# Performance work log

Measured on AMD Instinct MI355X. Metric: run time of the kernel, lower is better.

Reference implementation:

```python
import jax, jax.numpy as jnp
import numpy as np

SEQ, BATCH, D, N = 256, 4, 512, 32768
TEMP = 0.5


def setup_inputs() -> dict:
    key = jax.random.key(0)
    ks = jax.random.split(key, 16)
    d = D
    # xavier_uniform with gain 1/sqrt(2) for square [d,d]: limit = gain*sqrt(6/(d+d))
    lim_t = (1.0 / np.sqrt(2.0)) * np.sqrt(6.0 / (d + d))
    lim_g1 = np.sqrt(6.0 / (2 * d + d))  # default kaiming-ish scale approximated by xavier
    lim_g2 = np.sqrt(6.0 / (d + 1))
    inp = {
        "q": jax.random.normal(ks[0], (SEQ, BATCH, D), dtype=jnp.float32),
        "prev_layer_output": jax.random.normal(ks[1], (SEQ, BATCH, D), dtype=jnp.float32),
        "Wq": jax.random.uniform(ks[2], (D, D), jnp.float32, -lim_t, lim_t),
        "bq": jnp.zeros((D,), jnp.float32),
        "Wk": jax.random.uniform(ks[3], (D, D), jnp.float32, -lim_t, lim_t),
        "bk": jnp.zeros((D,), jnp.float32),
        "Wv": jax.random.uniform(ks[4], (D, D), jnp.float32, -lim_t, lim_t),
        "bv": jnp.zeros((D,), jnp.float32),
        "Wg1": jax.random.uniform(ks[5], (D, 2 * D), jnp.float32, -lim_g1, lim_g1),
        "bg1": jnp.zeros((D,), jnp.float32),
        "Wg2": jax.random.uniform(ks[6], (1, D), jnp.float32, -lim_g2, lim_g2),
        "bg2": jnp.zeros((1,), jnp.float32),
        "dstore_k": jax.random.normal(ks[7], (N, D), dtype=jnp.float32),
        "dstore_v": jax.random.normal(ks[8], (N, D), dtype=jnp.float32),
    }
    return inp


def reference(q, prev_layer_output, Wq, bq, Wk, bk, Wv, bv, Wg1, bg1, Wg2, bg2, dstore_k, dstore_v):
    # [S,B,D] -> [B,S,D]
    qb = jnp.transpose(q, (1, 0, 2))
    prevb = jnp.transpose(prev_layer_output, (1, 0, 2))
    # enable_tune projections
    _q = qb @ Wq.T + bq                      # [B,S,D]
    _k = dstore_k @ Wk.T + bk                # [N,D]
    _v = dstore_v @ Wv.T + bv                # [N,D]
    _q = _q * (D ** -0.5)
    # attention over datastore, temperature-scaled softmax
    logits = jnp.einsum("bsd,nd->bsn", _q, _k) / TEMP  # [B,S,N]
    w = jax.nn.softmax(logits, axis=-1)
    attn = jnp.einsum("bsn,nd->bsd", w, _v)            # [B,S,D]
    # gated residual fusion
    cat = jnp.concatenate([attn, prevb], axis=-1)      # [B,S,2D]
    h = jax.nn.relu(cat @ Wg1.T + bg1)                 # [B,S,D]
    sigma = jax.nn.sigmoid(h @ Wg2.T + bg2)            # [B,S,1]
    res = attn * sigma + prevb * (1.0 - sigma)
    return jnp.transpose(res, (1, 0, 2))               # [S,B,D]
```

## Files before the change

### kernel.cpp

```cpp
#include <hip/hip_runtime.h>
#include <hip/hip_bf16.h>
#include <cstdint>
#include <cstddef>


typedef unsigned short u16;
typedef u16    u16x8 __attribute__((ext_vector_type(8)));
typedef u16    u16x4 __attribute__((ext_vector_type(4)));
typedef __bf16 bf16x8 __attribute__((ext_vector_type(8)));
typedef float  f32x4 __attribute__((ext_vector_type(4)));

#define MFMA16(a, b, c) __builtin_amdgcn_mfma_f32_16x16x32_bf16( \
    __builtin_bit_cast(bf16x8, (a)), __builtin_bit_cast(bf16x8, (b)), (c), 0, 0, 0)

__device__ __forceinline__ u16 f2bf(float f) {
  unsigned u = __builtin_bit_cast(unsigned, f);
  u += 0x7fffu + ((u >> 16) & 1u);
  return (u16)(u >> 16);
}

__global__ __launch_bounds__(256) void prep_cvt(const float* __restrict__ src,
                                                u16* __restrict__ dst) {
  size_t i = ((size_t)blockIdx.x * 256 + threadIdx.x) * 4;
  float4 v = *(const float4*)(src + i);
  u16x4 o = {f2bf(v.x), f2bf(v.y), f2bf(v.z), f2bf(v.w)};
  *(u16x4*)(dst + i) = o;
}

__global__ __launch_bounds__(256) void prep_vt(const float* __restrict__ v,
                                               u16* __restrict__ vt) {
  __shared__ u16 Lt[64 * 72];
  const int n0 = blockIdx.x * 64, d0 = blockIdx.y * 64;
  const int t = threadIdx.x;
  const int n = t >> 2, c4 = t & 3;
#pragma unroll
  for (int i = 0; i < 4; i++) {
    int col = (c4 + 4 * i) * 4;
    float4 x = *(const float4*)(v + (size_t)(n0 + n) * 512 + d0 + col);
    Lt[(col + 0) * 72 + n] = f2bf(x.x);
    Lt[(col + 1) * 72 + n] = f2bf(x.y);
    Lt[(col + 2) * 72 + n] = f2bf(x.z);
    Lt[(col + 3) * 72 + n] = f2bf(x.w);
  }
  __syncthreads();
#pragma unroll
  for (int u = 0; u < 2; u++) {
    int unit = t + 256 * u;
    int d = unit >> 3, un = unit & 7;
    *(u16x8*)(vt + (size_t)(d0 + d) * 32768 + n0 + un * 8) =
        *(const u16x8*)&Lt[d * 72 + un * 8];
  }
}

template <bool TRANSB, bool CONCAT, bool RELU, bool OUTBF16, bool ROWSCALE,
          bool CQ, bool GATE, int KK>
__global__ __launch_bounds__(256, 2) void gemm64(
    const float* __restrict__ A, const float* __restrict__ A2,
    const float* __restrict__ B, const float* __restrict__ bias,
    const float* __restrict__ lvec, const float* __restrict__ bkv,
    const float* __restrict__ wg2, float alpha, void* __restrict__ Cv,
    float* __restrict__ cqout, float* __restrict__ sdot) {
  __shared__ u16 As[64 * 72];
  __shared__ u16 Bs[64 * 72];
  const int tid = threadIdx.x;
  const int w = tid >> 6, lane = tid & 63, quad = lane >> 4, l15 = lane & 15;
  const int m0 = blockIdx.y * 64, n0 = blockIdx.x * 64;
  const int arow = tid >> 2, ac4 = tid & 3;
  float rs = 1.0f;
  if (ROWSCALE) rs = 1.0f / lvec[m0 + arow];
  const bool docq = CQ && (blockIdx.x == 0);
  float cqacc = 0.f;
  const f32x4 fzero = {0.f, 0.f, 0.f, 0.f};
  f32x4 acc[4];
#pragma unroll
  for (int i = 0; i < 4; i++) acc[i] = fzero;

  float4 ra[4], rb[4], rk[4];
  auto loadA = [&](int k0) {
    const float* src;
    if (CONCAT)
      src = (k0 < 512) ? (A + (size_t)(m0 + arow) * 512 + k0)
                       : (A2 + (size_t)(m0 + arow) * 512 + (k0 - 512));
    else
      src = A + (size_t)(m0 + arow) * KK + k0;
#pragma unroll
    for (int i = 0; i < 4; i++) ra[i] = *(const float4*)(src + (ac4 + 4 * i) * 4);
  };
  auto loadB = [&](int k0) {
    const float* src = TRANSB ? (B + (size_t)(n0 + arow) * KK + k0)
                              : (B + (size_t)(k0 + arow) * 512 + n0);
#pragma unroll
    for (int i = 0; i < 4; i++) rb[i] = *(const float4*)(src + (ac4 + 4 * i) * 4);
  };
  auto loadK = [&](int k0) {
#pragma unroll
    for (int i = 0; i < 4; i++) rk[i] = *(const float4*)(bkv + k0 + (ac4 + 4 * i) * 4);
  };

  loadA(0); loadB(0);
  if (docq) loadK(0);
#pragma unroll
  for (int k0 = 0; k0 < KK; k0 += 64) {
    __syncthreads();
#pragma unroll
    for (int i = 0; i < 4; i++) {
      int col = (ac4 + 4 * i) * 4;
      float4 x = ra[i];
      if (ROWSCALE) { x.x *= rs; x.y *= rs; x.z *= rs; x.w *= rs; }
      u16x4 oa = {f2bf(x.x), f2bf(x.y), f2bf(x.z), f2bf(x.w)};
      *(u16x4*)&As[arow * 72 + col] = oa;
      float4 y = rb[i];
      if (TRANSB) {
        u16x4 ob = {f2bf(y.x), f2bf(y.y), f2bf(y.z), f2bf(y.w)};
        *(u16x4*)&Bs[arow * 72 + col] = ob;
      } else {
        Bs[(col + 0) * 72 + arow] = f2bf(y.x);
        Bs[(col + 1) * 72 + arow] = f2bf(y.y);
        Bs[(col + 2) * 72 + arow] = f2bf(y.z);
        Bs[(col + 3) * 72 + arow] = f2bf(y.w);
      }
      if (docq)
        cqacc += ra[i].x * rk[i].x + ra[i].y * rk[i].y + ra[i].z * rk[i].z +
                 ra[i].w * rk[i].w;
    }
    if (k0 + 64 < KK) {
      loadA(k0 + 64); loadB(k0 + 64);
      if (docq) loadK(k0 + 64);
    }
    __syncthreads();
#pragma unroll
    for (int ks = 0; ks < 2; ks++) {
      u16x8 af = *(const u16x8*)&As[(w * 16 + l15) * 72 + ks * 32 + quad * 8];
#pragma unroll
      for (int nt = 0; nt < 4; nt++) {
        u16x8 bf = *(const u16x8*)&Bs[(nt * 16 + l15) * 72 + ks * 32 + quad * 8];
        acc[nt] = MFMA16(af, bf, acc[nt]);
      }
    }
  }

  if (docq) {
    cqacc += __shfl_xor(cqacc, 1, 64);
    cqacc += __shfl_xor(cqacc, 2, 64);
    if (ac4 == 0) cqout[m0 + arow] = alpha * cqacc;
  }
  if (GATE) {
    float part[4] = {0.f, 0.f, 0.f, 0.f};
#pragma unroll
    for (int nt = 0; nt < 4; nt++) {
      int col = n0 + nt * 16 + l15;
      float b = bias[col], wv = wg2[col];
#pragma unroll
      for (int i = 0; i < 4; i++) {
        float y = fmaxf((acc[nt][i] + b) * alpha, 0.f);
        part[i] += y * wv;
      }
    }
#pragma unroll
    for (int i = 0; i < 4; i++) {
      float v = part[i];
      v += __shfl_xor(v, 1, 64); v += __shfl_xor(v, 2, 64);
      v += __shfl_xor(v, 4, 64); v += __shfl_xor(v, 8, 64);
      if (l15 == 0) atomicAdd(&sdot[m0 + w * 16 + quad * 4 + i], v);
    }
  } else {
#pragma unroll
    for (int nt = 0; nt < 4; nt++) {
      int col = n0 + nt * 16 + l15;
      float b = bias ? bias[col] : 0.f;
#pragma unroll
      for (int i = 0; i < 4; i++) {
        int row = m0 + w * 16 + quad * 4 + i;
        float y = (acc[nt][i] + b) * alpha;
        if (RELU) y = fmaxf(y, 0.f);
        if (OUTBF16)
          ((u16*)Cv)[(size_t)row * 512 + col] = f2bf(y);
        else
          ((float*)Cv)[(size_t)row * 512 + col] = y;
      }
    }
  }
}

__global__ __launch_bounds__(512, 2) void flash(
    const u16* __restrict__ kbf,
    const u16* __restrict__ vt,
    const u16* __restrict__ q2,
    const float* __restrict__ cq,
    float* __restrict__ racc,
    float* __restrict__ lacc) {
  __shared__ u16 Ks[32 * 520];
  __shared__ u16 Es[2][64 * 40];
  const int tid = threadIdx.x;
  const int w = tid >> 6, lane = tid & 63, quad = lane >> 4, l15 = lane & 15;
  const int bx = blockIdx.x;
  const int xcd = bx & 7, idx = bx >> 3;
  const int qt = idx & 15, nh2 = idx >> 4;
  const int rowbase = xcd * 4096 + nh2 * 2048;
  const int qbase = qt * 64;
  const int qg = w >> 1, nh = w & 1;
  const int colb = w * 64;

  u16x8 qf[16];
  {
    const u16* qp = q2 + (size_t)(qbase + qg * 16 + l15) * 512 + quad * 8;
#pragma unroll
    for (int ks = 0; ks < 16; ks++) qf[ks] = *(const u16x8*)(qp + ks * 32);
  }
  float cq4[4];
#pragma unroll
  for (int i = 0; i < 4; i++) cq4[i] = cq[qbase + qg * 16 + quad * 4 + i];
  float lp[4] = {0.f, 0.f, 0.f, 0.f};
  const f32x4 fzero = {0.f, 0.f, 0.f, 0.f};
  f32x4 acc[4][4];
#pragma unroll
  for (int a = 0; a < 4; a++)
#pragma unroll
    for (int b = 0; b < 4; b++) acc[a][b] = fzero;

  u16x8 st[4];
  u16x8 bvp[4];
#pragma unroll
  for (int u = 0; u < 4; u++) {
    int flat = tid + u * 512;
    st[u] = *(const u16x8*)(kbf + (size_t)(rowbase + (flat >> 6)) * 512 + (flat & 63) * 8);
  }

#pragma unroll 1
  for (int sub = 0; sub < 64; ++sub) {
    const int n0 = rowbase + sub * 32;
    __syncthreads();
#pragma unroll
    for (int u = 0; u < 4; u++) {
      int flat = tid + u * 512;
      *(u16x8*)&Ks[(flat >> 6) * 520 + (flat & 63) * 8] = st[u];
    }
    if (sub + 1 < 64) {
      int n1 = n0 + 32;
#pragma unroll
      for (int u = 0; u < 4; u++) {
        int flat = tid + u * 512;
        st[u] = *(const u16x8*)(kbf + (size_t)(n1 + (flat >> 6)) * 512 + (flat & 63) * 8);
      }
    }
    if (sub > 0) {
      const u16* eb = Es[(sub - 1) & 1];
      u16x8 ef[4];
#pragma unroll
      for (int q2i = 0; q2i < 4; q2i++)
        ef[q2i] = *(const u16x8*)&eb[(q2i * 16 + l15) * 40 + quad * 8];
#pragma unroll
      for (int ct = 0; ct < 4; ct++)
#pragma unroll
        for (int q2i = 0; q2i < 4; q2i++)
          acc[q2i][ct] = MFMA16(ef[q2i], bvp[ct], acc[q2i][ct]);
    }
    __syncthreads();
#pragma unroll
    for (int ct = 0; ct < 4; ct++)
      bvp[ct] = *(const u16x8*)(vt + (size_t)(colb + ct * 16 + l15) * 32768 + n0 + quad * 8);
    f32x4 s = fzero;
#pragma unroll
    for (int ks = 0; ks < 16; ks++) {
      u16x8 bfg = *(const u16x8*)&Ks[(nh * 16 + l15) * 520 + ks * 32 + quad * 8];
      s = MFMA16(qf[ks], bfg, s);
    }
    u16* ew = Es[sub & 1];
#pragma unroll
    for (int i = 0; i < 4; i++) {
      float e = __expf(s[i] + cq4[i]);
      lp[i] += e;
      ew[(qg * 16 + quad * 4 + i) * 40 + nh * 16 + l15] = f2bf(e);
    }
  }
  __syncthreads();
  {
    const u16* eb = Es[1];
    u16x8 ef[4];
#pragma unroll
    for (int q2i = 0; q2i < 4; q2i++)
      ef[q2i] = *(const u16x8*)&eb[(q2i * 16 + l15) * 40 + quad * 8];
#pragma unroll
    for (int ct = 0; ct < 4; ct++)
#pragma unroll
      for (int q2i = 0; q2i < 4; q2i++)
        acc[q2i][ct] = MFMA16(ef[q2i], bvp[ct], acc[q2i][ct]);
  }
#pragma unroll
  for (int q2i = 0; q2i < 4; q2i++)
#pragma unroll
    for (int ct = 0; ct < 4; ct++) {
      int col = colb + ct * 16 + l15;
#pragma unroll
      for (int i = 0; i < 4; i++) {
        int row = qbase + q2i * 16 + quad * 4 + i;
        atomicAdd(&racc[(size_t)row * 512 + col], acc[q2i][ct][i]);
      }
    }
#pragma unroll
  for (int i = 0; i < 4; i++) {
    float v = lp[i];
#pragma unroll
    for (int off = 1; off < 16; off <<= 1) v += __shfl_xor(v, off, 64);
    if (l15 == 0) atomicAdd(&lacc[qbase + qg * 16 + quad * 4 + i], v);
  }
}

__global__ __launch_bounds__(128) void finalize(
    const float* __restrict__ sdot, const float* __restrict__ bg2,
    const float* __restrict__ attn, const float* __restrict__ prev,
    float* __restrict__ out) {
  int r = blockIdx.x, t = threadIdx.x;
  float sg = 1.f / (1.f + __expf(-(sdot[r] + bg2[0])));
  float4 a = ((const float4*)(attn + (size_t)r * 512))[t];
  float4 p = ((const float4*)(prev + (size_t)r * 512))[t];
  float4 o = {a.x * sg + p.x * (1.f - sg), a.y * sg + p.y * (1.f - sg),
              a.z * sg + p.z * (1.f - sg), a.w * sg + p.w * (1.f - sg)};
  ((float4*)(out + (size_t)r * 512))[t] = o;
}

extern "C" void kernel_launch(void* const* d_in, const int* in_sizes, int n_in,
                              void* d_out, int out_size, void* d_ws, size_t ws_size,
                              hipStream_t stream) {
  const float* q    = (const float*)d_in[0];
  const float* prev = (const float*)d_in[1];
  const float* Wq   = (const float*)d_in[2];
  const float* bq   = (const float*)d_in[3];
  const float* Wk   = (const float*)d_in[4];
  const float* bk   = (const float*)d_in[5];
  const float* Wv   = (const float*)d_in[6];
  const float* bv   = (const float*)d_in[7];
  const float* Wg1  = (const float*)d_in[8];
  const float* bg1  = (const float*)d_in[9];
  const float* Wg2  = (const float*)d_in[10];
  const float* bg2  = (const float*)d_in[11];
  const float* dk   = (const float*)d_in[12];
  const float* dv   = (const float*)d_in[13];
  float* out = (float*)d_out;

  char* ws = (char*)d_ws;
  u16*   kbf  = (u16*)(ws);
  u16*   vt   = (u16*)(ws + 33554432);
  float* racc = (float*)(ws + 67108864);
  float* lacc = (float*)(ws + 69206016);
  float* sdot = (float*)(ws + 69210112);
  float* cqv  = (float*)(ws + 69214208);
  u16*   q2   = (u16*)(ws + 69218304);
  float* q1   = (float*)(ws + 70266880);
  float* attn = (float*)(ws + 72364032);

  prep_cvt<<<16384, 256, 0, stream>>>(dk, kbf);
  prep_vt<<<dim3(512, 8), 256, 0, stream>>>(dv, vt);
  gemm64<true, false, false, false, false, false, false, 512>
      <<<dim3(8, 16), 256, 0, stream>>>(q, nullptr, Wq, bq, nullptr, nullptr,
                                        nullptr, 0.044194173824159216f, q1,
                                        nullptr, nullptr);
  gemm64<false, false, false, true, false, true, false, 512>
      <<<dim3(8, 16), 256, 0, stream>>>(q1, nullptr, Wk, nullptr, nullptr, bk,
                                        nullptr, 2.0f, q2, cqv, nullptr);
  hipMemsetAsync(racc, 0, 2105344, stream);
  flash<<<256, 512, 0, stream>>>(kbf, vt, q2, cqv, racc, lacc);
  gemm64<true, false, false, false, true, false, false, 512>
      <<<dim3(8, 16), 256, 0, stream>>>(racc, nullptr, Wv, bv, lacc, nullptr,
                                        nullptr, 1.0f, attn, nullptr, nullptr);
  gemm64<true, true, true, false, false, false, true, 1024>
      <<<dim3(8, 16), 256, 0, stream>>>(attn, prev, Wg1, bg1, nullptr, nullptr,
                                        Wg2, 1.0f, nullptr, nullptr, sdot);
  finalize<<<1024, 128, 0, stream>>>(sdot, bg2, attn, prev, out);
}
```

Measured before the change: 435.4 us.

## Fuse prep kernels, precompute Wq·Wk, and restructure flash with LDS DMA double-buffering

```diff
diff --git a/kernel.cpp b/kernel.cpp
--- a/kernel.cpp
+++ b/kernel.cpp
@@ -13,53 +13,90 @@
 #define MFMA16(a, b, c) __builtin_amdgcn_mfma_f32_16x16x32_bf16( \
     __builtin_bit_cast(bf16x8, (a)), __builtin_bit_cast(bf16x8, (b)), (c), 0, 0, 0)
 
+#define AS1 __attribute__((address_space(1)))
+#define AS3 __attribute__((address_space(3)))
+
 __device__ __forceinline__ u16 f2bf(float f) {
   unsigned u = __builtin_bit_cast(unsigned, f);
   u += 0x7fffu + ((u >> 16) & 1u);
   return (u16)(u >> 16);
 }
 
-__global__ __launch_bounds__(256) void prep_cvt(const float* __restrict__ src,
-                                                u16* __restrict__ dst) {
-  size_t i = ((size_t)blockIdx.x * 256 + threadIdx.x) * 4;
-  float4 v = *(const float4*)(src + i);
-  u16x4 o = {f2bf(v.x), f2bf(v.y), f2bf(v.z), f2bf(v.w)};
-  *(u16x4*)(dst + i) = o;
-}
-
-__global__ __launch_bounds__(256) void prep_vt(const float* __restrict__ v,
-                                               u16* __restrict__ vt) {
-  __shared__ u16 Lt[64 * 72];
-  const int n0 = blockIdx.x * 64, d0 = blockIdx.y * 64;
-  const int t = threadIdx.x;
-  const int n = t >> 2, c4 = t & 3;
-#pragma unroll
-  for (int i = 0; i < 4; i++) {
-    int col = (c4 + 4 * i) * 4;
-    float4 x = *(const float4*)(v + (size_t)(n0 + n) * 512 + d0 + col);
-    Lt[(col + 0) * 72 + n] = f2bf(x.x);
-    Lt[(col + 1) * 72 + n] = f2bf(x.y);
-    Lt[(col + 2) * 72 + n] = f2bf(x.z);
-    Lt[(col + 3) * 72 + n] = f2bf(x.w);
-  }
-  __syncthreads();
-#pragma unroll
-  for (int u = 0; u < 2; u++) {
-    int unit = t + 256 * u;
-    int d = unit >> 3, un = unit & 7;
-    *(u16x8*)(vt + (size_t)(d0 + d) * 32768 + n0 + un * 8) =
-        *(const u16x8*)&Lt[d * 72 + un * 8];
-  }
-}
-
-template <bool TRANSB, bool CONCAT, bool RELU, bool OUTBF16, bool ROWSCALE,
-          bool CQ, bool GATE, int KK>
+__device__ __forceinline__ void dma16(const u16* g, u16* l) {
+  __builtin_amdgcn_global_load_lds((const AS1 unsigned int*)g,
+                                   (AS3 unsigned int*)l, 16, 0, 0);
+}
+
+__global__ __launch_bounds__(256) void prep_all(
+    const float* __restrict__ dk, const float* __restrict__ dv,
+    const float* __restrict__ Wq, const float* __restrict__ Wk,
+    const float* __restrict__ bk, const float* __restrict__ bq,
+    u16* __restrict__ kbf, u16* __restrict__ vt, float* __restrict__ zbase,
+    float* __restrict__ cqvec, float* __restrict__ b2pre,
+    float* __restrict__ cq0) {
+  const int bx = blockIdx.x, t = threadIdx.x;
+  if (bx < 4096) {
+    __shared__ u16 Lt[64 * 72];
+    const int n0 = (bx & 511) * 64, d0 = (bx >> 9) * 64;
+    const int n = t >> 2, c4 = t & 3;
+#pragma unroll
+    for (int i = 0; i < 4; i++) {
+      int col = (c4 + 4 * i) * 4;
+      float4 x = *(const float4*)(dv + (size_t)(n0 + n) * 512 + d0 + col);
+      Lt[(col + 0) * 72 + n] = f2bf(x.x);
+      Lt[(col + 1) * 72 + n] = f2bf(x.y);
+      Lt[(col + 2) * 72 + n] = f2bf(x.z);
+      Lt[(col + 3) * 72 + n] = f2bf(x.w);
+    }
+    __syncthreads();
+#pragma unroll
+    for (int u = 0; u < 2; u++) {
+      int unit = t + 256 * u;
+      int d = unit >> 3, un = unit & 7;
+      *(u16x8*)(vt + (size_t)(d0 + d) * 32768 + n0 + un * 8) =
+          *(const u16x8*)&Lt[d * 72 + un * 8];
+    }
+  } else if (bx < 8192) {
+    const int j = bx - 4096;
+    size_t i0 = ((size_t)j * 256 + t) * 16;
+#pragma unroll
+    for (int u = 0; u < 4; u++) {
+      float4 v = *(const float4*)(dk + i0 + u * 4);
+      u16x4 o = {f2bf(v.x), f2bf(v.y), f2bf(v.z), f2bf(v.w)};
+      *(u16x4*)(kbf + i0 + u * 4) = o;
+    }
+    int zi = j * 256 + t;
+    if (zi < 131584) ((float4*)zbase)[zi] = make_float4(0.f, 0.f, 0.f, 0.f);
+  } else if (bx < 8194) {
+    int e = (bx - 8192) * 256 + t;
+    float s1 = 0.f, s2 = 0.f;
+    for (int d = 0; d < 512; d++) {
+      s1 += bk[d] * Wq[d * 512 + e];
+      s2 += bq[d] * Wk[d * 512 + e];
+    }
+    cqvec[e] = s1;
+    b2pre[e] = s2;
+  } else {
+    __shared__ float red[4];
+    float s = 0.f;
+    for (int d = t; d < 512; d += 256) s += bq[d] * bk[d];
+#pragma unroll
+    for (int off = 32; off; off >>= 1) s += __shfl_down(s, off, 64);
+    if ((t & 63) == 0) red[t >> 6] = s;
+    __syncthreads();
+    if (t == 0) cq0[0] = 0.0883883476483184f * (red[0] + red[1] + red[2] + red[3]);
+  }
+}
+
+template <bool TRANSA, bool TRANSB, bool CONCAT, bool RELU, bool OUTBF16,
+          bool ROWSCALE, bool CQ, bool GATE, int KK>
 __global__ __launch_bounds__(256, 2) void gemm64(
     const float* __restrict__ A, const float* __restrict__ A2,
     const float* __restrict__ B, const float* __restrict__ bias,
     const float* __restrict__ lvec, const float* __restrict__ bkv,
     const float* __restrict__ wg2, float alpha, void* __restrict__ Cv,
-    float* __restrict__ cqout, float* __restrict__ sdot) {
+    float* __restrict__ cqout, const float* __restrict__ cq0buf,
+    float* __restrict__ sdot) {
   __shared__ u16 As[64 * 72];
   __shared__ u16 Bs[64 * 72];
   const int tid = threadIdx.x;
@@ -78,7 +115,9 @@
   float4 ra[4], rb[4], rk[4];
   auto loadA = [&](int k0) {
     const float* src;
-    if (CONCAT)
+    if (TRANSA)
+      src = A + (size_t)(k0 + arow) * 512 + m0;
+    else if (CONCAT)
       src = (k0 < 512) ? (A + (size_t)(m0 + arow) * 512 + k0)
                        : (A2 + (size_t)(m0 + arow) * 512 + (k0 - 512));
     else
@@ -97,7 +136,8 @@
     for (int i = 0; i < 4; i++) rk[i] = *(const float4*)(bkv + k0 + (ac4 + 4 * i) * 4);
   };
 
-  loadA(0); loadB(0);
+  loadA(0);
+  loadB(0);
   if (docq) loadK(0);
 #pragma unroll
   for (int k0 = 0; k0 < KK; k0 += 64) {
@@ -107,8 +147,15 @@
       int col = (ac4 + 4 * i) * 4;
       float4 x = ra[i];
       if (ROWSCALE) { x.x *= rs; x.y *= rs; x.z *= rs; x.w *= rs; }
-      u16x4 oa = {f2bf(x.x), f2bf(x.y), f2bf(x.z), f2bf(x.w)};
-      *(u16x4*)&As[arow * 72 + col] = oa;
+      if (TRANSA) {
+        As[(col + 0) * 72 + arow] = f2bf(x.x);
+        As[(col + 1) * 72 + arow] = f2bf(x.y);
+        As[(col + 2) * 72 + arow] = f2bf(x.z);
+        As[(col + 3) * 72 + arow] = f2bf(x.w);
+      } else {
+        u16x4 oa = {f2bf(x.x), f2bf(x.y), f2bf(x.z), f2bf(x.w)};
+        *(u16x4*)&As[arow * 72 + col] = oa;
+      }
       float4 y = rb[i];
       if (TRANSB) {
         u16x4 ob = {f2bf(y.x), f2bf(y.y), f2bf(y.z), f2bf(y.w)};
@@ -124,7 +171,8 @@
                  ra[i].w * rk[i].w;
     }
     if (k0 + 64 < KK) {
-      loadA(k0 + 64); loadB(k0 + 64);
+      loadA(k0 + 64);
+      loadB(k0 + 64);
       if (docq) loadK(k0 + 64);
     }
     __syncthreads();
@@ -142,7 +190,7 @@
   if (docq) {
     cqacc += __shfl_xor(cqacc, 1, 64);
     cqacc += __shfl_xor(cqacc, 2, 64);
-    if (ac4 == 0) cqout[m0 + arow] = alpha * cqacc;
+    if (ac4 == 0) cqout[m0 + arow] = alpha * cqacc + cq0buf[0];
   }
   if (GATE) {
     float part[4] = {0.f, 0.f, 0.f, 0.f};
@@ -151,10 +199,7 @@
       int col = n0 + nt * 16 + l15;
       float b = bias[col], wv = wg2[col];
 #pragma unroll
-      for (int i = 0; i < 4; i++) {
-        float y = fmaxf((acc[nt][i] + b) * alpha, 0.f);
-        part[i] += y * wv;
-      }
+      for (int i = 0; i < 4; i++) part[i] += fmaxf((acc[nt][i] + b) * alpha, 0.f) * wv;
     }
 #pragma unroll
     for (int i = 0; i < 4; i++) {
@@ -189,102 +234,94 @@
     const float* __restrict__ cq,
     float* __restrict__ racc,
     float* __restrict__ lacc) {
-  __shared__ u16 Ks[32 * 520];
-  __shared__ u16 Es[2][64 * 40];
+  __shared__ u16 Ks[2][64 * 520];
+  __shared__ u16 Es[2][64 * 72];
   const int tid = threadIdx.x;
   const int w = tid >> 6, lane = tid & 63, quad = lane >> 4, l15 = lane & 15;
   const int bx = blockIdx.x;
   const int xcd = bx & 7, idx = bx >> 3;
-  const int qt = idx & 15, nh2 = idx >> 4;
-  const int rowbase = xcd * 4096 + nh2 * 2048;
+  const int qt = idx & 15, half = idx >> 4;
+  const int rowbase = (xcd * 2 + half) * 2048;
   const int qbase = qt * 64;
-  const int qg = w >> 1, nh = w & 1;
+  const int qh = w & 1, nq = w >> 1;
   const int colb = w * 64;
 
-  u16x8 qf[16];
-  {
-    const u16* qp = q2 + (size_t)(qbase + qg * 16 + l15) * 512 + quad * 8;
-#pragma unroll
-    for (int ks = 0; ks < 16; ks++) qf[ks] = *(const u16x8*)(qp + ks * 32);
-  }
-  float cq4[4];
-#pragma unroll
-  for (int i = 0; i < 4; i++) cq4[i] = cq[qbase + qg * 16 + quad * 4 + i];
-  float lp[4] = {0.f, 0.f, 0.f, 0.f};
+  u16x8 qf[2][16];
+  float cqs[2];
+#pragma unroll
+  for (int st = 0; st < 2; st++) {
+    const u16* qp = q2 + (size_t)(qbase + qh * 32 + st * 16 + l15) * 512 + quad * 8;
+#pragma unroll
+    for (int ks = 0; ks < 16; ks++) qf[st][ks] = *(const u16x8*)(qp + ks * 32);
+    cqs[st] = cq[qbase + qh * 32 + st * 16 + l15];
+  }
   const f32x4 fzero = {0.f, 0.f, 0.f, 0.f};
   f32x4 acc[4][4];
 #pragma unroll
   for (int a = 0; a < 4; a++)
 #pragma unroll
     for (int b = 0; b < 4; b++) acc[a][b] = fzero;
-
-  u16x8 st[4];
-  u16x8 bvp[4];
-#pragma unroll
-  for (int u = 0; u < 4; u++) {
-    int flat = tid + u * 512;
-    st[u] = *(const u16x8*)(kbf + (size_t)(rowbase + (flat >> 6)) * 512 + (flat & 63) * 8);
-  }
+  float lp[2] = {0.f, 0.f};
+
+  auto dma_sub = [&](int sub) {
+    u16* dst = &Ks[sub & 1][(w * 8) * 520];
+    const u16* g = kbf + (size_t)(rowbase + sub * 64 + w * 8) * 512 + lane * 8;
+#pragma unroll
+    for (int j = 0; j < 8; j++) dma16(g + (size_t)j * 512, dst + j * 520);
+  };
+
+  dma_sub(0);
+  __builtin_amdgcn_s_waitcnt(0);
+  __syncthreads();
 
 #pragma unroll 1
-  for (int sub = 0; sub < 64; ++sub) {
-    const int n0 = rowbase + sub * 32;
+  for (int sub = 0; sub < 32; ++sub) {
+    const int buf = sub & 1;
+    const int n0 = rowbase + sub * 64;
+    if (sub + 1 < 32) dma_sub(sub + 1);
+    u16x8 bvp[2][4];
+#pragma unroll
+    for (int nk = 0; nk < 2; nk++)
+#pragma unroll
+      for (int ct = 0; ct < 4; ct++)
+        bvp[nk][ct] = *(const u16x8*)(vt + (size_t)(colb + ct * 16 + l15) * 32768 +
+                                      n0 + nk * 32 + quad * 8);
+    f32x4 sa[2][2];
+    sa[0][0] = fzero; sa[0][1] = fzero; sa[1][0] = fzero; sa[1][1] = fzero;
+#pragma unroll
+    for (int ks = 0; ks < 16; ks++) {
+      u16x8 af = *(const u16x8*)&Ks[buf][(nq * 16 + l15) * 520 + ks * 32 + quad * 8];
+      sa[0][ks & 1] = MFMA16(af, qf[0][ks], sa[0][ks & 1]);
+      sa[1][ks & 1] = MFMA16(af, qf[1][ks], sa[1][ks & 1]);
+    }
+#pragma unroll
+    for (int st = 0; st < 2; st++) {
+      f32x4 sv = sa[st][0] + sa[st][1];
+      u16x4 pk;
+      float ls = 0.f;
+#pragma unroll
+      for (int i = 0; i < 4; i++) {
+        float e = __expf(sv[i] + cqs[st]);
+        ls += e;
+        pk[i] = f2bf(e);
+      }
+      lp[st] += ls;
+      *(u16x4*)&Es[buf][(qh * 32 + st * 16 + l15) * 72 + nq * 16 + quad * 4] = pk;
+    }
+    __builtin_amdgcn_s_waitcnt(0);
     __syncthreads();
 #pragma unroll
-    for (int u = 0; u < 4; u++) {
-      int flat = tid + u * 512;
-      *(u16x8*)&Ks[(flat >> 6) * 520 + (flat & 63) * 8] = st[u];
-    }
-    if (sub + 1 < 64) {
-      int n1 = n0 + 32;
-#pragma unroll
-      for (int u = 0; u < 4; u++) {
-        int flat = tid + u * 512;
-        st[u] = *(const u16x8*)(kbf + (size_t)(n1 + (flat >> 6)) * 512 + (flat & 63) * 8);
-      }
-    }
-    if (sub > 0) {
-      const u16* eb = Es[(sub - 1) & 1];
+    for (int nk = 0; nk < 2; nk++) {
       u16x8 ef[4];
 #pragma unroll
       for (int q2i = 0; q2i < 4; q2i++)
-        ef[q2i] = *(const u16x8*)&eb[(q2i * 16 + l15) * 40 + quad * 8];
+        ef[q2i] = *(const u16x8*)&Es[buf][(q2i * 16 + l15) * 72 + nk * 32 + quad * 8];
 #pragma unroll
       for (int ct = 0; ct < 4; ct++)
 #pragma unroll
         for (int q2i = 0; q2i < 4; q2i++)
-          acc[q2i][ct] = MFMA16(ef[q2i], bvp[ct], acc[q2i][ct]);
-    }
-    __syncthreads();
-#pragma unroll
-    for (int ct = 0; ct < 4; ct++)
-      bvp[ct] = *(const u16x8*)(vt + (size_t)(colb + ct * 16 + l15) * 32768 + n0 + quad * 8);
-    f32x4 s = fzero;
-#pragma unroll
-    for (int ks = 0; ks < 16; ks++) {
-      u16x8 bfg = *(const u16x8*)&Ks[(nh * 16 + l15) * 520 + ks * 32 + quad * 8];
-      s = MFMA16(qf[ks], bfg, s);
-    }
-    u16* ew = Es[sub & 1];
-#pragma unroll
-    for (int i = 0; i < 4; i++) {
-      float e = __expf(s[i] + cq4[i]);
-      lp[i] += e;
-      ew[(qg * 16 + quad * 4 + i) * 40 + nh * 16 + l15] = f2bf(e);
-    }
-  }
-  __syncthreads();
-  {
-    const u16* eb = Es[1];
-    u16x8 ef[4];
-#pragma unroll
-    for (int q2i = 0; q2i < 4; q2i++)
-      ef[q2i] = *(const u16x8*)&eb[(q2i * 16 + l15) * 40 + quad * 8];
-#pragma unroll
-    for (int ct = 0; ct < 4; ct++)
-#pragma unroll
-      for (int q2i = 0; q2i < 4; q2i++)
-        acc[q2i][ct] = MFMA16(ef[q2i], bvp[ct], acc[q2i][ct]);
+          acc[q2i][ct] = MFMA16(ef[q2i], bvp[nk][ct], acc[q2i][ct]);
+    }
   }
 #pragma unroll
   for (int q2i = 0; q2i < 4; q2i++)
@@ -298,11 +335,11 @@
       }
     }
 #pragma unroll
-  for (int i = 0; i < 4; i++) {
-    float v = lp[i];
-#pragma unroll
-    for (int off = 1; off < 16; off <<= 1) v += __shfl_xor(v, off, 64);
-    if (l15 == 0) atomicAdd(&lacc[qbase + qg * 16 + quad * 4 + i], v);
+  for (int st = 0; st < 2; st++) {
+    float v = lp[st];
+    v += __shfl_xor(v, 16, 64);
+    v += __shfl_xor(v, 32, 64);
+    if (quad == 0) atomicAdd(&lacc[qbase + qh * 32 + st * 16 + l15], v);
   }
 }
 
@@ -339,32 +376,37 @@
   float* out = (float*)d_out;
 
   char* ws = (char*)d_ws;
-  u16*   kbf  = (u16*)(ws);
-  u16*   vt   = (u16*)(ws + 33554432);
-  float* racc = (float*)(ws + 67108864);
-  float* lacc = (float*)(ws + 69206016);
-  float* sdot = (float*)(ws + 69210112);
-  float* cqv  = (float*)(ws + 69214208);
-  u16*   q2   = (u16*)(ws + 69218304);
-  float* q1   = (float*)(ws + 70266880);
-  float* attn = (float*)(ws + 72364032);
-
-  prep_cvt<<<16384, 256, 0, stream>>>(dk, kbf);
-  prep_vt<<<dim3(512, 8), 256, 0, stream>>>(dv, vt);
-  gemm64<true, false, false, false, false, false, false, 512>
-      <<<dim3(8, 16), 256, 0, stream>>>(q, nullptr, Wq, bq, nullptr, nullptr,
-                                        nullptr, 0.044194173824159216f, q1,
-                                        nullptr, nullptr);
-  gemm64<false, false, false, true, false, true, false, 512>
-      <<<dim3(8, 16), 256, 0, stream>>>(q1, nullptr, Wk, nullptr, nullptr, bk,
-                                        nullptr, 2.0f, q2, cqv, nullptr);
-  hipMemsetAsync(racc, 0, 2105344, stream);
+  u16*   kbf   = (u16*)(ws);
+  u16*   vt    = (u16*)(ws + 33554432);
+  float* racc  = (float*)(ws + 67108864);
+  float* lacc  = (float*)(ws + 69206016);
+  float* sdot  = (float*)(ws + 69210112);
+  float* cqv   = (float*)(ws + 69214208);
+  u16*   q2    = (u16*)(ws + 69218304);
+  float* Wqk   = (float*)(ws + 70266880);
+  float* cqvec = (float*)(ws + 71315456);
+  float* b2pre = (float*)(ws + 71317504);
+  float* cq0   = (float*)(ws + 71319552);
+  float* attn  = (float*)(ws + 72364032);
+
+  prep_all<<<8195, 256, 0, stream>>>(dk, dv, Wq, Wk, bk, bq, kbf, vt, racc,
+                                     cqvec, b2pre, cq0);
+  gemm64<true, false, false, false, false, false, false, false, 512>
+      <<<dim3(8, 8), 256, 0, stream>>>(Wq, nullptr, Wk, nullptr, nullptr,
+                                       nullptr, nullptr, 1.0f, Wqk, nullptr,
+                                       nullptr, nullptr);
+  gemm64<false, false, false, false, true, false, true, false, 512>
+      <<<dim3(8, 16), 256, 0, stream>>>(q, nullptr, Wqk, b2pre, nullptr, cqvec,
+                                        nullptr, 0.0883883476483184f, q2, cqv,
+                                        cq0, nullptr);
   flash<<<256, 512, 0, stream>>>(kbf, vt, q2, cqv, racc, lacc);
-  gemm64<true, false, false, false, true, false, false, 512>
+  gemm64<false, true, false, false, false, true, false, false, 512>
       <<<dim3(8, 16), 256, 0, stream>>>(racc, nullptr, Wv, bv, lacc, nullptr,
-                                        nullptr, 1.0f, attn, nullptr, nullptr);
-  gemm64<true, true, true, false, false, false, true, 1024>
+                                        nullptr, 1.0f, attn, nullptr, nullptr,
+                                        nullptr);
+  gemm64<false, true, true, true, false, false, false, true, 1024>
       <<<dim3(8, 16), 256, 0, stream>>>(attn, prev, Wg1, bg1, nullptr, nullptr,
-                                        Wg2, 1.0f, nullptr, nullptr, sdot);
+                                        Wg2, 1.0f, nullptr, nullptr, nullptr,
+                                        sdot);
   finalize<<<1024, 128, 0, stream>>>(sdot, bg2, attn, prev, out);
 }
```

Result: slower. 475.8 us (+9.3%).
